# Kernel tuning notes

Measured on AMD Instinct MI355X. Metric: run time of the kernel, lower is better.

The kernel has to match this reference:

```python
import jax, jax.numpy as jnp
import numpy as np

N = 100000
E = 600000
H = 128  # embedding_size
DEPTH = 6


def setup_inputs() -> dict:
    key = jax.random.key(0)
    ks = jax.random.split(key, 12)
    X = jax.random.normal(ks[0], (N, 3), dtype=jnp.float32)
    edge_index = jax.random.randint(ks[1], (2, E), 0, N, dtype=jnp.int64)
    s = 1.0 / np.sqrt(H)
    W0 = jax.random.uniform(ks[2], (H, 3), jnp.float32, -s, s)
    b0 = jax.random.uniform(ks[3], (H,), jnp.float32, -s, s)
    W_ih = jax.random.uniform(ks[4], (3 * H, H), jnp.float32, -s, s)
    W_hh = jax.random.uniform(ks[5], (3 * H, H), jnp.float32, -s, s)
    b_ih = jax.random.uniform(ks[6], (3 * H,), jnp.float32, -s, s)
    b_hh = jax.random.uniform(ks[7], (3 * H,), jnp.float32, -s, s)
    Wm1 = jax.random.uniform(ks[8], (H // 2, H), jnp.float32, -s, s)
    bm1 = jax.random.uniform(ks[9], (H // 2,), jnp.float32, -s, s)
    Wm2 = jax.random.uniform(ks[10], (1, H // 2), jnp.float32, -s, s)
    bm2 = jax.random.uniform(ks[11], (1,), jnp.float32, -s, s)
    return {"X": X, "edge_index": edge_index, "W0": W0, "b0": b0,
            "W_ih": W_ih, "W_hh": W_hh, "b_ih": b_ih, "b_hh": b_hh,
            "Wm1": Wm1, "bm1": bm1, "Wm2": Wm2, "bm2": bm2}


def _gcn_agg(h, row, col, norm):
    # out[i] = sum_{e: col[e]==i} norm[e] * h[row[e]]
    msgs = norm[:, None] * h[row]          # [E, H]
    return jax.ops.segment_sum(msgs, col, num_segments=N)


def _gru_cell(x, h, W_ih, W_hh, b_ih, b_hh):
    gx = x @ W_ih.T + b_ih                 # [N, 3H]
    gh = h @ W_hh.T + b_hh                 # [N, 3H]
    xr, xz, xn = jnp.split(gx, 3, axis=1)
    hr, hz, hn = jnp.split(gh, 3, axis=1)
    r = jax.nn.sigmoid(xr + hr)
    z = jax.nn.sigmoid(xz + hz)
    n = jnp.tanh(xn + r * hn)
    return (1.0 - z) * n + z * h


def reference(X, edge_index, W0, b0, W_ih, W_hh, b_ih, b_hh, Wm1, bm1, Wm2, bm2):
    row, col = edge_index[0], edge_index[1]
    # degree over concat(row, col), +1, inv-sqrt with inf->0
    ones = jnp.ones((2 * E,), dtype=X.dtype)
    deg = jax.ops.segment_sum(ones, jnp.concatenate([row, col]), num_segments=N) + 1.0
    deg_inv_sqrt = deg ** -0.5
    deg_inv_sqrt = jnp.where(jnp.isinf(deg_inv_sqrt), 0.0, deg_inv_sqrt)
    norm = deg_inv_sqrt[row] * deg_inv_sqrt[col]  # [E]

    h = jax.nn.leaky_relu(X @ W0.T + b0, negative_slope=0.01)  # [N, H]
    h_max = jnp.full_like(h, -jnp.inf)
    for _ in range(DEPTH - 1):
        h_aggre = _gcn_agg(h, row, col, norm)
        h = _gru_cell(h_aggre, h, W_ih, W_hh, b_ih, b_hh)
        h_max = jnp.maximum(h_max, h)

    hid = jax.nn.leaky_relu(h_max @ Wm1.T + bm1, negative_slope=0.01)
    out = hid @ Wm2.T + bm2                # [N, 1]
    return jnp.squeeze(out, axis=-1)       # [N]
```

## Files before the change

### kernel.cpp

```cpp
#include <hip/hip_runtime.h>

#define Nn 100000
#define Ee 600000
#define Hh 128
#define NP 100096
#define NT (NP / 64)

typedef float f32x4 __attribute__((ext_vector_type(4)));
typedef _Float16 f16x8 __attribute__((ext_vector_type(8)));

static __device__ __forceinline__ float sigmoidf_(float x) {
  return 1.0f / (1.0f + __expf(-x));
}
static __device__ __forceinline__ float tanh_fast(float x) {
  return 1.0f - 2.0f / (__expf(2.0f * x) + 1.0f);
}
static __device__ __forceinline__ int swz(int u) {
  return u ^ (((u >> 11) & 3) << 4);
}

__global__ void count_kernel(const int* __restrict__ ei, int* __restrict__ degi,
                             int* __restrict__ cnt) {
  int e = blockIdx.x * 256 + threadIdx.x;
  if (e >= Ee) return;
  int r = ei[e], c = ei[Ee + e];
  atomicAdd(&degi[r], 1);
  atomicAdd(&degi[c], 1);
  atomicAdd(&cnt[c], 1);
}

__global__ void scan_partial(const int* __restrict__ cnt, const int* __restrict__ degi,
                             float* __restrict__ dis, int* __restrict__ bsum) {
  __shared__ int s[256];
  int i = blockIdx.x * 256 + threadIdx.x;
  s[threadIdx.x] = (i < Nn) ? cnt[i] : 0;
  if (i < Nn) dis[i] = rsqrtf((float)degi[i] + 1.0f);
  __syncthreads();
  for (int off = 128; off > 0; off >>= 1) {
    if (threadIdx.x < off) s[threadIdx.x] += s[threadIdx.x + off];
    __syncthreads();
  }
  if (threadIdx.x == 0) bsum[blockIdx.x] = s[0];
}

__global__ void scan_bsums(const int* __restrict__ bsum, int* __restrict__ bpre, int nb) {
  __shared__ int s[512];
  int t = threadIdx.x;
  s[t] = (t < nb) ? bsum[t] : 0;
  __syncthreads();
  for (int off = 1; off < 512; off <<= 1) {
    int u = (t >= off) ? s[t - off] : 0;
    __syncthreads();
    s[t] += u;
    __syncthreads();
  }
  if (t < nb) bpre[t] = (t == 0) ? 0 : s[t - 1];
}

__global__ void scan_final(const int* __restrict__ cnt, const int* __restrict__ bpre,
                           int* __restrict__ rowptr, int* __restrict__ cursor) {
  __shared__ int s[256];
  int t = threadIdx.x;
  int i = blockIdx.x * 256 + t;
  int v = (i < Nn) ? cnt[i] : 0;
  s[t] = v;
  __syncthreads();
  for (int off = 1; off < 256; off <<= 1) {
    int u = (t >= off) ? s[t - off] : 0;
    __syncthreads();
    s[t] += u;
    __syncthreads();
  }
  int excl = s[t] - v;
  int base = bpre[blockIdx.x];
  if (i < Nn) { rowptr[i] = base + excl; cursor[i] = base + excl; }
  if (i == Nn - 1) rowptr[Nn] = base + excl + v;
}

__global__ void fill_kernel(const int* __restrict__ ei, const float* __restrict__ dis,
                            int* __restrict__ cursor, int* __restrict__ csr_src,
                            float* __restrict__ csr_w) {
  int e = blockIdx.x * 256 + threadIdx.x;
  if (e >= Ee) return;
  int r = ei[e], c = ei[Ee + e];
  int p = atomicAdd(&cursor[c], 1);
  csr_src[p] = r;
  csr_w[p] = dis[r] * dis[c];
}

__global__ void pack_kernel(const float* __restrict__ Wih, const float* __restrict__ Whh,
                            _Float16* __restrict__ Bhi, _Float16* __restrict__ Blo) {
  int t = blockIdx.x * 256 + threadIdx.x;
  if (t >= 8 * 24 * 4 * 16) return;
  int c16 = t & 15;
  int g = (t >> 4) & 3;
  int fid = (t >> 6) % 24;
  int kc = t / (24 * 64);
  int gate = fid >> 3, f = fid & 7;
  int c = f * 16 + c16;
  int wrow = gate * 128 + c;
  size_t base = (size_t)t * 8;
#pragma unroll
  for (int j = 0; j < 8; ++j) {
    int k = kc * 32 + g * 8 + j;
    float v = (k < 128) ? Wih[wrow * 128 + k] : Whh[wrow * 128 + (k - 128)];
    _Float16 hi = (_Float16)v;
    Bhi[base + j] = hi;
    Blo[base + j] = (_Float16)(v - (float)hi);
  }
}

__global__ void pack_mlp(const float* __restrict__ Wm1, _Float16* __restrict__ Bh,
                         _Float16* __restrict__ Bl) {
  int t = blockIdx.x * 256 + threadIdx.x;
  if (t >= 1024) return;
  int c16 = t & 15;
  int g = (t >> 4) & 3;
  int cf = (t >> 6) & 3;
  int kc = t >> 8;
  int c = cf * 16 + c16;
  size_t base = (size_t)t * 8;
#pragma unroll
  for (int j = 0; j < 8; ++j) {
    int k = kc * 32 + g * 8 + j;
    float v = Wm1[c * 128 + k];
    _Float16 hi = (_Float16)v;
    Bh[base + j] = hi;
    Bl[base + j] = (_Float16)(v - (float)hi);
  }
}

__global__ void h0_kernel(const float* __restrict__ X, const float* __restrict__ W0,
                          const float* __restrict__ b0, _Float16* __restrict__ H0) {
  int t = blockIdx.x * 256 + threadIdx.x;
  int i = t >> 7, d = t & 127;
  if (i >= NP) return;
  float v = 0.0f;
  if (i < Nn) {
    float x0 = X[i * 3 + 0], x1 = X[i * 3 + 1], x2 = X[i * 3 + 2];
    v = fmaf(x0, W0[d * 3 + 0], fmaf(x1, W0[d * 3 + 1], fmaf(x2, W0[d * 3 + 2], b0[d])));
    v = v > 0.0f ? v : 0.01f * v;
  }
  H0[(size_t)i * Hh + d] = (_Float16)v;
}

#define DO_GATE_AG(GB, ACC)                                                           \
  {                                                                                   \
    size_t boff = (((size_t)(kc * 24 + (GB)*8 + wave) * 4 + g) * 16 + c16) * 8;       \
    f16x8 bH = *(const f16x8*)(Bhi + boff);                                           \
    f16x8 bL = *(const f16x8*)(Blo + boff);                                           \
    _Pragma("unroll") for (int rf = 0; rf < 4; ++rf)                                  \
        ACC[rf] = __builtin_amdgcn_mfma_f32_16x16x32_f16(aH[rf], bH, ACC[rf], 0, 0, 0); \
    _Pragma("unroll") for (int rf = 0; rf < 4; ++rf)                                  \
        ACC[rf] = __builtin_amdgcn_mfma_f32_16x16x32_f16(aH[rf], bL, ACC[rf], 0, 0, 0); \
    _Pragma("unroll") for (int rf = 0; rf < 4; ++rf)                                  \
        ACC[rf] = __builtin_amdgcn_mfma_f32_16x16x32_f16(aL[rf], bH, ACC[rf], 0, 0, 0); \
  }

#define DO_GATE_H(GB, ACC)                                                            \
  {                                                                                   \
    size_t boff = (((size_t)(kc * 24 + (GB)*8 + wave) * 4 + g) * 16 + c16) * 8;       \
    f16x8 bH = *(const f16x8*)(Bhi + boff);                                           \
    f16x8 bL = *(const f16x8*)(Blo + boff);                                           \
    _Pragma("unroll") for (int rf = 0; rf < 4; ++rf)                                  \
        ACC[rf] = __builtin_amdgcn_mfma_f32_16x16x32_f16(aE[rf], bH, ACC[rf], 0, 0, 0); \
    _Pragma("unroll") for (int rf = 0; rf < 4; ++rf)                                  \
        ACC[rf] = __builtin_amdgcn_mfma_f32_16x16x32_f16(aE[rf], bL, ACC[rf], 0, 0, 0); \
  }

#define GRU_BODY                                                                      \
  const int tid = threadIdx.x;                                                        \
  const int tile = blockIdx.x;                                                        \
  const long rowbase = (long)tile * 64;                                               \
  const int local = tid >> 3;                                                         \
  const int sub = tid & 7;                                                            \
  const int eg = sub & 1;                                                             \
  const int dg = sub >> 1;                                                            \
  const int rf0 = local >> 4, c16l = local & 15;                                      \
  const int lwr = dg * 2048 + rf0 * 512 + c16l * 8;                                   \
  {                                                                                   \
    const long node = rowbase + local;                                                \
    float acc[32];                                                                    \
    _Pragma("unroll") for (int m = 0; m < 32; ++m) acc[m] = 0.0f;                     \
    if (node < Nn) {                                                                  \
      const int eEnd = rowptr[node + 1];                                              \
      int e = rowptr[node] + eg;                                                      \
      const _Float16* hb = Hp + dg * 32;                                              \
      for (; e + 2 < eEnd; e += 4) {                                                  \
        const int s0 = csr_src[e], s1 = csr_src[e + 2];                               \
        const float w0 = csr_w[e], w1 = csr_w[e + 2];                                 \
        const f16x8* p0 = (const f16x8*)(hb + (size_t)s0 * Hh);                       \
        const f16x8* p1 = (const f16x8*)(hb + (size_t)s1 * Hh);                       \
        f16x8 va[4], vb[4];                                                           \
        _Pragma("unroll") for (int q = 0; q < 4; ++q) va[q] = p0[q];                  \
        _Pragma("unroll") for (int q = 0; q < 4; ++q) vb[q] = p1[q];                  \
        _Pragma("unroll") for (int q = 0; q < 4; ++q)                                 \
            _Pragma("unroll") for (int m = 0; m < 8; ++m)                             \
                acc[q * 8 + m] = fmaf(w1, (float)vb[q][m],                            \
                                      fmaf(w0, (float)va[q][m], acc[q * 8 + m]));     \
      }                                                                               \
      if (e < eEnd) {                                                                 \
        const int s0 = csr_src[e];                                                    \
        const float w0 = csr_w[e];                                                    \
        const f16x8* p0 = (const f16x8*)(hb + (size_t)s0 * Hh);                       \
        f16x8 va[4];                                                                  \
        _Pragma("unroll") for (int q = 0; q < 4; ++q) va[q] = p0[q];                  \
        _Pragma("unroll") for (int q = 0; q < 4; ++q)                                 \
            _Pragma("unroll") for (int m = 0; m < 8; ++m)                             \
                acc[q * 8 + m] = fmaf(w0, (float)va[q][m], acc[q * 8 + m]);           \
      }                                                                               \
    }                                                                                 \
    _Pragma("unroll") for (int m = 0; m < 32; ++m) acc[m] += __shfl_xor(acc[m], 1);   \
    if (eg == 0) {                                                                    \
      _Pragma("unroll") for (int g2 = 0; g2 < 4; ++g2) {                              \
        f16x8 vh, vl;                                                                 \
        _Pragma("unroll") for (int j = 0; j < 8; ++j) {                               \
          float v = acc[g2 * 8 + j];                                                  \
          _Float16 hi = (_Float16)v;                                                  \
          vh[j] = hi;                                                                 \
          vl[j] = (_Float16)(v - (float)hi);                                          \
        }                                                                             \
        const int o = swz(lwr + g2 * 128);                                            \
        *(f16x8*)(SH + o) = vh;                                                       \
        *(f16x8*)(SL + o) = vl;                                                       \
      }                                                                               \
    }                                                                                 \
  }                                                                                   \
  __syncthreads();                                                                    \
  const int wave = tid >> 6, lane = tid & 63;                                         \
  const int g = lane >> 4, c16 = lane & 15;                                           \
  const int lbase = g * 128 + c16 * 8;                                                \
  f32x4 accR[4], accZ[4], accXN[4], accHN[4];                                         \
  _Pragma("unroll") for (int rf = 0; rf < 4; ++rf) {                                  \
    accR[rf] = (f32x4){0.f, 0.f, 0.f, 0.f};                                           \
    accZ[rf] = (f32x4){0.f, 0.f, 0.f, 0.f};                                           \
    accXN[rf] = (f32x4){0.f, 0.f, 0.f, 0.f};                                          \
    accHN[rf] = (f32x4){0.f, 0.f, 0.f, 0.f};                                          \
  }                                                                                   \
  _Pragma("unroll") for (int kc = 0; kc < 4; ++kc) {                                  \
    f16x8 aH[4], aL[4];                                                               \
    _Pragma("unroll") for (int rf = 0; rf < 4; ++rf) {                                \
      int off = swz(kc * 2048 + rf * 512 + lbase);                                    \
      aH[rf] = *(const f16x8*)(SH + off);                                             \
      aL[rf] = *(const f16x8*)(SL + off);                                             \
    }                                                                                 \
    DO_GATE_AG(0, accR)                                                               \
    DO_GATE_AG(1, accZ)                                                               \
    DO_GATE_AG(2, accXN)                                                              \
  }                                                                                   \
  __syncthreads();                                                                    \
  {                                                                                   \
    const _Float16* p = Hp + (size_t)(rowbase + local) * Hh + dg * 32 + eg * 16;      \
    f16x8 v0 = *(const f16x8*)p;                                                      \
    f16x8 v1 = *(const f16x8*)(p + 8);                                                \
    *(f16x8*)(SH + swz(lwr + (eg * 2 + 0) * 128)) = v0;                               \
    *(f16x8*)(SH + swz(lwr + (eg * 2 + 1) * 128)) = v1;                               \
  }                                                                                   \
  __syncthreads();                                                                    \
  _Pragma("unroll") for (int kc = 4; kc < 8; ++kc) {                                  \
    f16x8 aE[4];                                                                      \
    _Pragma("unroll") for (int rf = 0; rf < 4; ++rf) {                                \
      int off = swz((kc - 4) * 2048 + rf * 512 + lbase);                              \
      aE[rf] = *(const f16x8*)(SH + off);                                             \
    }                                                                                 \
    DO_GATE_H(0, accR)                                                                \
    DO_GATE_H(1, accZ)                                                                \
    DO_GATE_H(2, accHN)                                                               \
  }                                                                                   \
  const int c = wave * 16 + c16;                                                      \
  const float br = bih[c] + bhh[c];                                                   \
  const float bz = bih[128 + c] + bhh[128 + c];                                       \
  const float bxn = bih[256 + c];                                                     \
  const float bhn = bhh[256 + c];                                                     \
  const int kcs = c >> 5;                                                             \
  const int gs = (c >> 3) & 3;                                                        \
  const int js = c & 7;

__global__ __launch_bounds__(512, 4) void gcn_gru_fused(
    const _Float16* __restrict__ Hp, _Float16* __restrict__ Hn,
    const int* __restrict__ csr_src, const float* __restrict__ csr_w,
    const int* __restrict__ rowptr,
    const _Float16* __restrict__ Bhi, const _Float16* __restrict__ Blo,
    const float* __restrict__ bih, const float* __restrict__ bhh) {
  __shared__ ushort SH[8192];
  __shared__ ushort SL[8192];
  GRU_BODY
#pragma unroll
  for (int rf = 0; rf < 4; ++rf) {
#pragma unroll
    for (int reg = 0; reg < 4; ++reg) {
      const int lr = g * 4 + reg;
      const int hoff = swz(kcs * 2048 + rf * 512 + gs * 128 + lr * 8 + js);
      float hold = (float)*(const _Float16*)&SH[hoff];
      float rr = sigmoidf_(accR[rf][reg] + br);
      float zz = sigmoidf_(accZ[rf][reg] + bz);
      float nn = tanh_fast(accXN[rf][reg] + bxn + rr * (accHN[rf][reg] + bhn));
      Hn[(size_t)(rowbase + rf * 16 + lr) * Hh + c] =
          (_Float16)((1.0f - zz) * nn + zz * hold);
    }
  }
}

__global__ __launch_bounds__(512, 4) void gcn_gru_last(
    const _Float16* __restrict__ Hp,
    const _Float16* __restrict__ Ha, const _Float16* __restrict__ Hb,
    const _Float16* __restrict__ Hc,
    const int* __restrict__ csr_src, const float* __restrict__ csr_w,
    const int* __restrict__ rowptr,
    const _Float16* __restrict__ Bhi, const _Float16* __restrict__ Blo,
    const float* __restrict__ bih, const float* __restrict__ bhh,
    const _Float16* __restrict__ Bmh, const _Float16* __restrict__ Bml,
    const float* __restrict__ bm1, const float* __restrict__ Wm2,
    const float* __restrict__ bm2, float* __restrict__ out) {
  __shared__ ushort SH[8192];
  __shared__ ushort SL[8192];
  __shared__ float red[8][64];
  GRU_BODY
#pragma unroll
  for (int rf = 0; rf < 4; ++rf) {
#pragma unroll
    for (int reg = 0; reg < 4; ++reg) {
      const int lr = g * 4 + reg;
      const int hoff = swz(kcs * 2048 + rf * 512 + gs * 128 + lr * 8 + js);
      float hold = (float)*(const _Float16*)&SH[hoff];
      float rr = sigmoidf_(accR[rf][reg] + br);
      float zz = sigmoidf_(accZ[rf][reg] + bz);
      float nn = tanh_fast(accXN[rf][reg] + bxn + rr * (accHN[rf][reg] + bhn));
      *(_Float16*)&SL[hoff] = (_Float16)((1.0f - zz) * nn + zz * hold);
    }
  }
  __syncthreads();

  {
    const size_t o = (size_t)(rowbase + local) * Hh + dg * 32 + eg * 16;
#pragma unroll
    for (int h2 = 0; h2 < 2; ++h2) {
      const int slot = swz(lwr + (eg * 2 + h2) * 128);
      f16x8 m = *(const f16x8*)(SL + slot);
      f16x8 v;
      v = *(const f16x8*)(Hp + o + h2 * 8);
#pragma unroll
      for (int mm = 0; mm < 8; ++mm) m[mm] = m[mm] > v[mm] ? m[mm] : v[mm];
      v = *(const f16x8*)(Ha + o + h2 * 8);
#pragma unroll
      for (int mm = 0; mm < 8; ++mm) m[mm] = m[mm] > v[mm] ? m[mm] : v[mm];
      v = *(const f16x8*)(Hb + o + h2 * 8);
#pragma unroll
      for (int mm = 0; mm < 8; ++mm) m[mm] = m[mm] > v[mm] ? m[mm] : v[mm];
      v = *(const f16x8*)(Hc + o + h2 * 8);
#pragma unroll
      for (int mm = 0; mm < 8; ++mm) m[mm] = m[mm] > v[mm] ? m[mm] : v[mm];
      *(f16x8*)(SH + slot) = m;
    }
  }
  __syncthreads();

  {
    const int cf = wave >> 1, kh = wave & 1;
    f32x4 macc[4];
#pragma unroll
    for (int rf = 0; rf < 4; ++rf) macc[rf] = (f32x4){0.f, 0.f, 0.f, 0.f};
#pragma unroll
    for (int q = 0; q < 2; ++q) {
      const int kc = kh * 2 + q;
      f16x8 aE[4];
#pragma unroll
      for (int rf = 0; rf < 4; ++rf) {
        int off = swz(kc * 2048 + rf * 512 + lbase);
        aE[rf] = *(const f16x8*)(SH + off);
      }
      size_t boff = (((size_t)(kc * 4 + cf) * 4 + g) * 16 + c16) * 8;
      f16x8 bH = *(const f16x8*)(Bmh + boff);
      f16x8 bL = *(const f16x8*)(Bml + boff);
#pragma unroll
      for (int rf = 0; rf < 4; ++rf)
        macc[rf] = __builtin_amdgcn_mfma_f32_16x16x32_f16(aE[rf], bH, macc[rf], 0, 0, 0);
#pragma unroll
      for (int rf = 0; rf < 4; ++rf)
        macc[rf] = __builtin_amdgcn_mfma_f32_16x16x32_f16(aE[rf], bL, macc[rf], 0, 0, 0);
    }
    const int hc = cf * 16 + c16;
    const float b1 = bm1[hc] * 0.5f;
    const float w2 = Wm2[hc];
#pragma unroll
    for (int rf = 0; rf < 4; ++rf) {
#pragma unroll
      for (int reg = 0; reg < 4; ++reg) {
        float v = macc[rf][reg];
#pragma unroll
        for (int off = 1; off < 16; off <<= 1) v += __shfl_xor(v, off);
        if (c16 == 0) red[wave][rf * 16 + g * 4 + reg] = v;
      }
    }
    (void)b1;
    (void)w2;
  }
  __syncthreads();
  if (tid < 64) {
    long row = rowbase + tid;
    if (row < Nn) out[row] = red[0][tid] + red[1][tid] + red[2][tid] + red[3][tid] +
                             red[4][tid] + red[5][tid] + red[6][tid] + red[7][tid];
  }
}

extern "C" void kernel_launch(void* const* d_in, const int* in_sizes, int n_in,
                              void* d_out, int out_size, void* d_ws, size_t ws_size,
                              hipStream_t stream);


__global__ __launch_bounds__(512, 4) void gcn_gru_last2(
    const _Float16* __restrict__ Hp, const _Float16* __restrict__ Ha,
    const _Float16* __restrict__ Hb, const _Float16* __restrict__ Hc,
    const int* __restrict__ csr_src, const float* __restrict__ csr_w,
    const int* __restrict__ rowptr,
    const _Float16* __restrict__ Bhi, const _Float16* __restrict__ Blo,
    const float* __restrict__ bih, const float* __restrict__ bhh,
    const _Float16* __restrict__ Bmh, const _Float16* __restrict__ Bml,
    const float* __restrict__ bm1, const float* __restrict__ Wm2,
    const float* __restrict__ bm2, float* __restrict__ out) {
  __shared__ ushort SH[8192];
  __shared__ ushort SL[8192];
  __shared__ float hid[64][65];
  GRU_BODY
#pragma unroll
  for (int rf = 0; rf < 4; ++rf) {
#pragma unroll
    for (int reg = 0; reg < 4; ++reg) {
      const int lr = g * 4 + reg;
      const int hoff = swz(kcs * 2048 + rf * 512 + gs * 128 + lr * 8 + js);
      float hold = (float)*(const _Float16*)&SH[hoff];
      float rr = sigmoidf_(accR[rf][reg] + br);
      float zz = sigmoidf_(accZ[rf][reg] + bz);
      float nn = tanh_fast(accXN[rf][reg] + bxn + rr * (accHN[rf][reg] + bhn));
      *(_Float16*)&SL[hoff] = (_Float16)((1.0f - zz) * nn + zz * hold);
    }
  }
  __syncthreads();

  {
    const size_t o = (size_t)(rowbase + local) * Hh + dg * 32 + eg * 16;
#pragma unroll
    for (int h2 = 0; h2 < 2; ++h2) {
      const int slot = swz(lwr + (eg * 2 + h2) * 128);
      f16x8 m = *(const f16x8*)(SL + slot);
      f16x8 v;
      v = *(const f16x8*)(Hp + o + h2 * 8);
#pragma unroll
      for (int mm = 0; mm < 8; ++mm) m[mm] = m[mm] > v[mm] ? m[mm] : v[mm];
      v = *(const f16x8*)(Ha + o + h2 * 8);
#pragma unroll
      for (int mm = 0; mm < 8; ++mm) m[mm] = m[mm] > v[mm] ? m[mm] : v[mm];
      v = *(const f16x8*)(Hb + o + h2 * 8);
#pragma unroll
      for (int mm = 0; mm < 8; ++mm) m[mm] = m[mm] > v[mm] ? m[mm] : v[mm];
      v = *(const f16x8*)(Hc + o + h2 * 8);
#pragma unroll
      for (int mm = 0; mm < 8; ++mm) m[mm] = m[mm] > v[mm] ? m[mm] : v[mm];
      *(f16x8*)(SH + slot) = m;
    }
  }
  __syncthreads();

  {
    const int cf = wave >> 1, kh = wave & 1;
    f32x4 macc[4];
#pragma unroll
    for (int rf = 0; rf < 4; ++rf) macc[rf] = (f32x4){0.f, 0.f, 0.f, 0.f};
#pragma unroll
    for (int q = 0; q < 2; ++q) {
      const int kc = kh * 2 + q;
      f16x8 aE[4];
#pragma unroll
      for (int rf = 0; rf < 4; ++rf) {
        int off = swz(kc * 2048 + rf * 512 + lbase);
        aE[rf] = *(const f16x8*)(SH + off);
      }
      size_t boff = (((size_t)(kc * 4 + cf) * 4 + g) * 16 + c16) * 8;
      f16x8 bH = *(const f16x8*)(Bmh + boff);
      f16x8 bL = *(const f16x8*)(Bml + boff);
#pragma unroll
      for (int rf = 0; rf < 4; ++rf)
        macc[rf] = __builtin_amdgcn_mfma_f32_16x16x32_f16(aE[rf], bH, macc[rf], 0, 0, 0);
#pragma unroll
      for (int rf = 0; rf < 4; ++rf)
        macc[rf] = __builtin_amdgcn_mfma_f32_16x16x32_f16(aE[rf], bL, macc[rf], 0, 0, 0);
    }
    const int hc = cf * 16 + c16;
#pragma unroll
    for (int rf = 0; rf < 4; ++rf)
#pragma unroll
      for (int reg = 0; reg < 4; ++reg) {
        const int row = rf * 16 + g * 4 + reg;
        if (kh == 0)
          hid[row][hc] = macc[rf][reg];
        else
          hid[row + 0][hc + 0] = hid[row][hc];
      }
    __syncthreads();
    if (kh == 1) {
#pragma unroll
      for (int rf = 0; rf < 4; ++rf)
#pragma unroll
        for (int reg = 0; reg < 4; ++reg) {
          const int row = rf * 16 + g * 4 + reg;
          hid[row][hc] += macc[rf][reg];
        }
    }
  }
  __syncthreads();

  if (tid < 64) {
    long row = rowbase + tid;
    if (row < Nn) {
      float s = 0.f;
#pragma unroll
      for (int cc = 0; cc < 64; ++cc) {
        float v = hid[tid][cc] + bm1[cc];
        v = v > 0.f ? v : 0.01f * v;
        s = fmaf(v, Wm2[cc], s);
      }
      out[row] = s + bm2[0];
    }
  }
}

extern "C" void kernel_launch(void* const* d_in, const int* in_sizes, int n_in,
                              void* d_out, int out_size, void* d_ws, size_t ws_size,
                              hipStream_t stream) {
  const float* X = (const float*)d_in[0];
  const int* ei = (const int*)d_in[1];
  const float* W0 = (const float*)d_in[2];
  const float* b0 = (const float*)d_in[3];
  const float* Wih = (const float*)d_in[4];
  const float* Whh = (const float*)d_in[5];
  const float* bih = (const float*)d_in[6];
  const float* bhh = (const float*)d_in[7];
  const float* Wm1 = (const float*)d_in[8];
  const float* bm1 = (const float*)d_in[9];
  const float* Wm2 = (const float*)d_in[10];
  const float* bm2 = (const float*)d_in[11];
  float* out = (float*)d_out;

  char* ws = (char*)d_ws;
  size_t off = 0;
  auto alloc = [&](size_t bytes) -> void* {
    void* p = ws + off;
    off = (off + bytes + 255) & ~(size_t)255;
    return p;
  };
  _Float16* Hs[5];
  for (int i = 0; i < 5; ++i) Hs[i] = (_Float16*)alloc((size_t)NP * Hh * 2);
  _Float16* Bhi = (_Float16*)alloc((size_t)8 * 24 * 4 * 16 * 8 * 2);
  _Float16* Blo = (_Float16*)alloc((size_t)8 * 24 * 4 * 16 * 8 * 2);
  _Float16* Bmh = (_Float16*)alloc((size_t)1024 * 8 * 2);
  _Float16* Bml = (_Float16*)alloc((size_t)1024 * 8 * 2);
  float* dis = (float*)alloc((size_t)Nn * 4);
  int* degi = (int*)alloc((size_t)Nn * 4);
  int* cnt = (int*)alloc((size_t)Nn * 4);
  int* rowptr = (int*)alloc((size_t)(Nn + 1) * 4);
  int* cursor = (int*)alloc((size_t)Nn * 4);
  int* bsum = (int*)alloc(512 * 4);
  int* bpre = (int*)alloc(512 * 4);
  int* csr_src = (int*)alloc((size_t)Ee * 4);
  float* csr_w = (float*)alloc((size_t)Ee * 4);
  (void)ws_size;
  (void)in_sizes;
  (void)n_in;
  (void)out_size;

  const int NB = (Nn + 255) / 256;
  const int EB = (Ee + 255) / 256;

  hipMemsetAsync(degi, 0, (size_t)Nn * 4, stream);
  hipMemsetAsync(cnt, 0, (size_t)Nn * 4, stream);
  count_kernel<<<EB, 256, 0, stream>>>(ei, degi, cnt);
  scan_partial<<<NB, 256, 0, stream>>>(cnt, degi, dis, bsum);
  scan_bsums<<<1, 512, 0, stream>>>(bsum, bpre, NB);
  scan_final<<<NB, 256, 0, stream>>>(cnt, bpre, rowptr, cursor);
  fill_kernel<<<EB, 256, 0, stream>>>(ei, dis, cursor, csr_src, csr_w);
  pack_kernel<<<48, 256, 0, stream>>>(Wih, Whh, Bhi, Blo);
  pack_mlp<<<4, 256, 0, stream>>>(Wm1, Bmh, Bml);
  h0_kernel<<<(NP * Hh) / 256, 256, 0, stream>>>(X, W0, b0, Hs[0]);

  for (int t = 1; t <= 4; ++t) {
    gcn_gru_fused<<<NT, 512, 0, stream>>>(Hs[t - 1], Hs[t], csr_src, csr_w,
                                          rowptr, Bhi, Blo, bih, bhh);
  }
  gcn_gru_last2<<<NT, 512, 0, stream>>>(Hs[4], Hs[1], Hs[2], Hs[3], csr_src, csr_w,
                                        rowptr, Bhi, Blo, bih, bhh, Bmh, Bml,
                                        bm1, Wm2, bm2, out);
}
```

Baseline: 569.6 us.

## Raise occupancy hints, alias hidden scratch into shared tiles, parallelize MLP head

Raises the launch_bounds minimum-blocks hint from 4 to 8 for the fused GRU kernels. This constrains registers per thread and may cause spills. The final kernel now reuses the SH/SL shared buffers for the hidden-layer scratch instead of a separate array, which cuts per-block LDS so more blocks can be resident. The final MLP reduction is spread across all 512 threads with shuffle reductions, where before only 64 threads looped serially. The dead unused gcn_gru_last kernel is also removed.

```diff
diff --git a/kernel.cpp b/kernel.cpp
--- a/kernel.cpp
+++ b/kernel.cpp
@@ -276,7 +276,7 @@
   const int gs = (c >> 3) & 3;                                                        \
   const int js = c & 7;
 
-__global__ __launch_bounds__(512, 4) void gcn_gru_fused(
+__global__ __launch_bounds__(512, 8) void gcn_gru_fused(
     const _Float16* __restrict__ Hp, _Float16* __restrict__ Hn,
     const int* __restrict__ csr_src, const float* __restrict__ csr_w,
     const int* __restrict__ rowptr,
@@ -301,114 +301,7 @@
   }
 }
 
-__global__ __launch_bounds__(512, 4) void gcn_gru_last(
-    const _Float16* __restrict__ Hp,
-    const _Float16* __restrict__ Ha, const _Float16* __restrict__ Hb,
-    const _Float16* __restrict__ Hc,
-    const int* __restrict__ csr_src, const float* __restrict__ csr_w,
-    const int* __restrict__ rowptr,
-    const _Float16* __restrict__ Bhi, const _Float16* __restrict__ Blo,
-    const float* __restrict__ bih, const float* __restrict__ bhh,
-    const _Float16* __restrict__ Bmh, const _Float16* __restrict__ Bml,
-    const float* __restrict__ bm1, const float* __restrict__ Wm2,
-    const float* __restrict__ bm2, float* __restrict__ out) {
-  __shared__ ushort SH[8192];
-  __shared__ ushort SL[8192];
-  __shared__ float red[8][64];
-  GRU_BODY
-#pragma unroll
-  for (int rf = 0; rf < 4; ++rf) {
-#pragma unroll
-    for (int reg = 0; reg < 4; ++reg) {
-      const int lr = g * 4 + reg;
-      const int hoff = swz(kcs * 2048 + rf * 512 + gs * 128 + lr * 8 + js);
-      float hold = (float)*(const _Float16*)&SH[hoff];
-      float rr = sigmoidf_(accR[rf][reg] + br);
-      float zz = sigmoidf_(accZ[rf][reg] + bz);
-      float nn = tanh_fast(accXN[rf][reg] + bxn + rr * (accHN[rf][reg] + bhn));
-      *(_Float16*)&SL[hoff] = (_Float16)((1.0f - zz) * nn + zz * hold);
-    }
-  }
-  __syncthreads();
-
-  {
-    const size_t o = (size_t)(rowbase + local) * Hh + dg * 32 + eg * 16;
-#pragma unroll
-    for (int h2 = 0; h2 < 2; ++h2) {
-      const int slot = swz(lwr + (eg * 2 + h2) * 128);
-      f16x8 m = *(const f16x8*)(SL + slot);
-      f16x8 v;
-      v = *(const f16x8*)(Hp + o + h2 * 8);
-#pragma unroll
-      for (int mm = 0; mm < 8; ++mm) m[mm] = m[mm] > v[mm] ? m[mm] : v[mm];
-      v = *(const f16x8*)(Ha + o + h2 * 8);
-#pragma unroll
-      for (int mm = 0; mm < 8; ++mm) m[mm] = m[mm] > v[mm] ? m[mm] : v[mm];
-      v = *(const f16x8*)(Hb + o + h2 * 8);
-#pragma unroll
-      for (int mm = 0; mm < 8; ++mm) m[mm] = m[mm] > v[mm] ? m[mm] : v[mm];
-      v = *(const f16x8*)(Hc + o + h2 * 8);
-#pragma unroll
-      for (int mm = 0; mm < 8; ++mm) m[mm] = m[mm] > v[mm] ? m[mm] : v[mm];
-      *(f16x8*)(SH + slot) = m;
-    }
-  }
-  __syncthreads();
-
-  {
-    const int cf = wave >> 1, kh = wave & 1;
-    f32x4 macc[4];
-#pragma unroll
-    for (int rf = 0; rf < 4; ++rf) macc[rf] = (f32x4){0.f, 0.f, 0.f, 0.f};
-#pragma unroll
-    for (int q = 0; q < 2; ++q) {
-      const int kc = kh * 2 + q;
-      f16x8 aE[4];
-#pragma unroll
-      for (int rf = 0; rf < 4; ++rf) {
-        int off = swz(kc * 2048 + rf * 512 + lbase);
-        aE[rf] = *(const f16x8*)(SH + off);
-      }
-      size_t boff = (((size_t)(kc * 4 + cf) * 4 + g) * 16 + c16) * 8;
-      f16x8 bH = *(const f16x8*)(Bmh + boff);
-      f16x8 bL = *(const f16x8*)(Bml + boff);
-#pragma unroll
-      for (int rf = 0; rf < 4; ++rf)
-        macc[rf] = __builtin_amdgcn_mfma_f32_16x16x32_f16(aE[rf], bH, macc[rf], 0, 0, 0);
-#pragma unroll
-      for (int rf = 0; rf < 4; ++rf)
-        macc[rf] = __builtin_amdgcn_mfma_f32_16x16x32_f16(aE[rf], bL, macc[rf], 0, 0, 0);
-    }
-    const int hc = cf * 16 + c16;
-    const float b1 = bm1[hc] * 0.5f;
-    const float w2 = Wm2[hc];
-#pragma unroll
-    for (int rf = 0; rf < 4; ++rf) {
-#pragma unroll
-      for (int reg = 0; reg < 4; ++reg) {
-        float v = macc[rf][reg];
-#pragma unroll
-        for (int off = 1; off < 16; off <<= 1) v += __shfl_xor(v, off);
-        if (c16 == 0) red[wave][rf * 16 + g * 4 + reg] = v;
-      }
-    }
-    (void)b1;
-    (void)w2;
-  }
-  __syncthreads();
-  if (tid < 64) {
-    long row = rowbase + tid;
-    if (row < Nn) out[row] = red[0][tid] + red[1][tid] + red[2][tid] + red[3][tid] +
-                             red[4][tid] + red[5][tid] + red[6][tid] + red[7][tid];
-  }
-}
-
-extern "C" void kernel_launch(void* const* d_in, const int* in_sizes, int n_in,
-                              void* d_out, int out_size, void* d_ws, size_t ws_size,
-                              hipStream_t stream);
-
-
-__global__ __launch_bounds__(512, 4) void gcn_gru_last2(
+__global__ __launch_bounds__(512, 8) void gcn_gru_last2(
     const _Float16* __restrict__ Hp, const _Float16* __restrict__ Ha,
     const _Float16* __restrict__ Hb, const _Float16* __restrict__ Hc,
     const int* __restrict__ csr_src, const float* __restrict__ csr_w,
@@ -418,9 +311,9 @@
     const _Float16* __restrict__ Bmh, const _Float16* __restrict__ Bml,
     const float* __restrict__ bm1, const float* __restrict__ Wm2,
     const float* __restrict__ bm2, float* __restrict__ out) {
-  __shared__ ushort SH[8192];
-  __shared__ ushort SL[8192];
-  __shared__ float hid[64][65];
+  __shared__ ushort S[16896];
+  ushort* SH = S;
+  ushort* SL = S + 8192;
   GRU_BODY
 #pragma unroll
   for (int rf = 0; rf < 4; ++rf) {
@@ -461,65 +354,67 @@
   }
   __syncthreads();
 
+  const int cf = wave >> 1, kh = wave & 1;
+  f32x4 macc[4];
+#pragma unroll
+  for (int rf = 0; rf < 4; ++rf) macc[rf] = (f32x4){0.f, 0.f, 0.f, 0.f};
+#pragma unroll
+  for (int q = 0; q < 2; ++q) {
+    const int kc = kh * 2 + q;
+    f16x8 aE[4];
+#pragma unroll
+    for (int rf = 0; rf < 4; ++rf) {
+      int off = swz(kc * 2048 + rf * 512 + lbase);
+      aE[rf] = *(const f16x8*)(SH + off);
+    }
+    size_t boff = (((size_t)(kc * 4 + cf) * 4 + g) * 16 + c16) * 8;
+    f16x8 bH = *(const f16x8*)(Bmh + boff);
+    f16x8 bL = *(const f16x8*)(Bml + boff);
+#pragma unroll
+    for (int rf = 0; rf < 4; ++rf)
+      macc[rf] = __builtin_amdgcn_mfma_f32_16x16x32_f16(aE[rf], bH, macc[rf], 0, 0, 0);
+#pragma unroll
+    for (int rf = 0; rf < 4; ++rf)
+      macc[rf] = __builtin_amdgcn_mfma_f32_16x16x32_f16(aE[rf], bL, macc[rf], 0, 0, 0);
+  }
+  __syncthreads();
+
+  float* hid = (float*)S;
+  const int hc = cf * 16 + c16;
+  if (kh == 0) {
+#pragma unroll
+    for (int rf = 0; rf < 4; ++rf)
+#pragma unroll
+      for (int reg = 0; reg < 4; ++reg)
+        hid[(rf * 16 + g * 4 + reg) * 66 + hc] = macc[rf][reg];
+  }
+  __syncthreads();
+  if (kh == 1) {
+#pragma unroll
+    for (int rf = 0; rf < 4; ++rf)
+#pragma unroll
+      for (int reg = 0; reg < 4; ++reg)
+        hid[(rf * 16 + g * 4 + reg) * 66 + hc] += macc[rf][reg];
+  }
+  __syncthreads();
+
   {
-    const int cf = wave >> 1, kh = wave & 1;
-    f32x4 macc[4];
-#pragma unroll
-    for (int rf = 0; rf < 4; ++rf) macc[rf] = (f32x4){0.f, 0.f, 0.f, 0.f};
-#pragma unroll
-    for (int q = 0; q < 2; ++q) {
-      const int kc = kh * 2 + q;
-      f16x8 aE[4];
-#pragma unroll
-      for (int rf = 0; rf < 4; ++rf) {
-        int off = swz(kc * 2048 + rf * 512 + lbase);
-        aE[rf] = *(const f16x8*)(SH + off);
-      }
-      size_t boff = (((size_t)(kc * 4 + cf) * 4 + g) * 16 + c16) * 8;
-      f16x8 bH = *(const f16x8*)(Bmh + boff);
-      f16x8 bL = *(const f16x8*)(Bml + boff);
-#pragma unroll
-      for (int rf = 0; rf < 4; ++rf)
-        macc[rf] = __builtin_amdgcn_mfma_f32_16x16x32_f16(aE[rf], bH, macc[rf], 0, 0, 0);
-#pragma unroll
-      for (int rf = 0; rf < 4; ++rf)
-        macc[rf] = __builtin_amdgcn_mfma_f32_16x16x32_f16(aE[rf], bL, macc[rf], 0, 0, 0);
-    }
-    const int hc = cf * 16 + c16;
-#pragma unroll
-    for (int rf = 0; rf < 4; ++rf)
-#pragma unroll
-      for (int reg = 0; reg < 4; ++reg) {
-        const int row = rf * 16 + g * 4 + reg;
-        if (kh == 0)
-          hid[row][hc] = macc[rf][reg];
-        else
-          hid[row + 0][hc + 0] = hid[row][hc];
-      }
-    __syncthreads();
-    if (kh == 1) {
-#pragma unroll
-      for (int rf = 0; rf < 4; ++rf)
-#pragma unroll
-        for (int reg = 0; reg < 4; ++reg) {
-          const int row = rf * 16 + g * 4 + reg;
-          hid[row][hc] += macc[rf][reg];
-        }
-    }
-  }
-  __syncthreads();
-
-  if (tid < 64) {
-    long row = rowbase + tid;
-    if (row < Nn) {
-      float s = 0.f;
-#pragma unroll
-      for (int cc = 0; cc < 64; ++cc) {
-        float v = hid[tid][cc] + bm1[cc];
-        v = v > 0.f ? v : 0.01f * v;
-        s = fmaf(v, Wm2[cc], s);
-      }
-      out[row] = s + bm2[0];
+    const int row = tid >> 3;
+    const int s8 = tid & 7;
+    float s = 0.f;
+#pragma unroll
+    for (int j = 0; j < 8; ++j) {
+      const int cc = s8 * 8 + j;
+      float v = hid[row * 66 + cc] + bm1[cc];
+      v = v > 0.f ? v : 0.01f * v;
+      s = fmaf(v, Wm2[cc], s);
+    }
+    s += __shfl_xor(s, 1);
+    s += __shfl_xor(s, 2);
+    s += __shfl_xor(s, 4);
+    if (s8 == 0) {
+      long grow = rowbase + row;
+      if (grow < Nn) out[grow] = s + bm2[0];
     }
   }
 }
```

Measured after the change: 2.255 ms. +295.9%, slower.
